# Kernel optimization log

Measured on AMD Instinct MI355X. Metric: run time of the kernel, lower is better.

The kernel has to match this reference:

```python
import jax, jax.numpy as jnp
import numpy as np

NUM_SEGMENTS = 4096  # number of graphs in the batch
E = 2097152          # number of edges
IN_CH = 64
HID_CH = 2 * IN_CH


def setup_inputs() -> dict:
    key = jax.random.key(0)
    k1, k2, k3, k4 = jax.random.split(key, 4)
    edge_attr = jax.random.normal(k1, (E, IN_CH), dtype=jnp.float32)
    batch = jnp.sort(jax.random.randint(k2, (E,), 0, NUM_SEGMENTS, dtype=jnp.int32))
    # MLP params: Linear(in, 2*in) -> ReLU -> Linear(2*in, 1)
    s1 = 1.0 / np.sqrt(IN_CH)
    s2 = 1.0 / np.sqrt(HID_CH)
    w1 = jax.random.uniform(k3, (IN_CH, HID_CH), jnp.float32, -s1, s1)
    b1 = jnp.zeros((HID_CH,), jnp.float32)
    w2 = jax.random.uniform(k4, (HID_CH, 1), jnp.float32, -s2, s2)
    b2 = jnp.zeros((1,), jnp.float32)
    return {"edge_attr": edge_attr, "w1": w1, "b1": b1, "w2": w2, "b2": b2, "batch": batch}


def reference(edge_attr, w1, b1, w2, b2, batch):
    # Tiny MLP scorer: [E, C] -> [E]
    h = jax.nn.relu(edge_attr @ w1 + b1)           # [E, 2C]
    score = (h @ w2 + b2).reshape(-1)              # [E]
    # Segment (per-graph) softmax keyed by `batch`, as in torch_geometric.utils.softmax
    seg_max = jax.ops.segment_max(score, batch, num_segments=NUM_SEGMENTS)  # [G]
    seg_max = jnp.where(jnp.isfinite(seg_max), seg_max, 0.0)  # empty segments
    ex = jnp.exp(score - seg_max[batch])           # [E]
    denom = jax.ops.segment_sum(ex, batch, num_segments=NUM_SEGMENTS)       # [G]
    return ex / (denom[batch] + 1e-16)
```

## Files before the change

kernel.cpp:

```cpp
#include <hip/hip_runtime.h>
#include <hip/hip_bf16.h>
#include <math.h>

typedef _Float16 half8  __attribute__((ext_vector_type(8)));
typedef __fp16   fp16x2 __attribute__((ext_vector_type(2)));
typedef float    floatx4 __attribute__((ext_vector_type(4)));

#define IN_CH 64
#define HID   128
#define NSEG  4096

__device__ __forceinline__ unsigned fkey(float s) {
    unsigned u = __float_as_uint(s);
    return (u & 0x80000000u) ? ~u : (u | 0x80000000u);
}
__device__ __forceinline__ float funkey(unsigned k) {
    unsigned u = (k & 0x80000000u) ? (k ^ 0x80000000u) : ~k;
    return __uint_as_float(u);
}

__global__ void init_seg(unsigned* __restrict__ segkey, float* __restrict__ denom) {
    int i = blockIdx.x * blockDim.x + threadIdx.x;
    if (i < NSEG) { segkey[i] = 0u; denom[i] = 0.0f; }
}

__global__ __launch_bounds__(256, 2) void mlp_score(
    const float* __restrict__ x, const float* __restrict__ w1,
    const float* __restrict__ b1, const float* __restrict__ w2,
    const float* __restrict__ b2, float* __restrict__ score, int E)
{
    __shared__ __align__(16) char smem[4 * 4 * 4096];

    const int tid  = threadIdx.x;
    const int lane = tid & 63;
    const int wid  = tid >> 6;
    const int g    = lane >> 4;
    const int l15  = lane & 15;
    const int ls4  = lane >> 4;

    half8 afr[2][8];
#pragma unroll
    for (int ks = 0; ks < 2; ++ks)
#pragma unroll
        for (int ct = 0; ct < 8; ++ct) {
            const float* wp = w1 + (size_t)(ks * 32 + g * 8) * HID + ct * 16 + l15;
            half8 h;
#pragma unroll
            for (int j = 0; j < 8; ++j) h[j] = (_Float16)wp[(size_t)j * HID];
            afr[ks][ct] = h;
        }

    floatx4 biasC[8], w2r[8];
#pragma unroll
    for (int ct = 0; ct < 8; ++ct)
#pragma unroll
        for (int r = 0; r < 4; ++r) {
            biasC[ct][r] = b1[ct * 16 + g * 4 + r];
            w2r[ct][r]   = w2[ct * 16 + g * 4 + r];
        }
    const float b2v = b2[0];

    const int nwtile = E >> 4;
    const int TOTW   = (int)gridDim.x * 4;
    const int gw     = blockIdx.x * 4 + wid;
    const int n      = nwtile / TOTW;
    const int rem    = nwtile - n * TOTW;

    char* lwave = smem + wid * 16384;
    const char* xb = (const char*)x;

    unsigned woff[4];
#pragma unroll
    for (int c = 0; c < 4; ++c) {
        int r = c * 4 + ls4;
        woff[c] = (unsigned)(r * 256 + ((l15 ^ r) & 15) * 16);
    }
    const unsigned roff = (unsigned)(l15 * 256 + (((2 * g) ^ l15) & 15) * 16);

    union H8 { half8 h8; fp16x2 h2[4]; };

#define STAGE(I) do {                                                          \
        size_t tb_ = (size_t)(gw + (I) * TOTW) * 4096;                         \
        char* lb_ = lwave + ((I) & 3) * 4096;                                  \
        __builtin_amdgcn_global_load_lds((const __attribute__((address_space(1))) void*)(xb + tb_ + woff[0]), (__attribute__((address_space(3))) void*)(lb_),        16, 0, 0); \
        __builtin_amdgcn_global_load_lds((const __attribute__((address_space(1))) void*)(xb + tb_ + woff[1]), (__attribute__((address_space(3))) void*)(lb_ + 1024), 16, 0, 0); \
        __builtin_amdgcn_global_load_lds((const __attribute__((address_space(1))) void*)(xb + tb_ + woff[2]), (__attribute__((address_space(3))) void*)(lb_ + 2048), 16, 0, 0); \
        __builtin_amdgcn_global_load_lds((const __attribute__((address_space(1))) void*)(xb + tb_ + woff[3]), (__attribute__((address_space(3))) void*)(lb_ + 3072), 16, 0, 0); \
    } while (0)

#define CORE(F0, F1, F2, F3, WT) do {                                          \
        H8 ub, uc;                                                             \
        ub.h2[0] = __builtin_amdgcn_cvt_pkrtz(F0[0], F0[1]);                   \
        ub.h2[1] = __builtin_amdgcn_cvt_pkrtz(F0[2], F0[3]);                   \
        ub.h2[2] = __builtin_amdgcn_cvt_pkrtz(F1[0], F1[1]);                   \
        ub.h2[3] = __builtin_amdgcn_cvt_pkrtz(F1[2], F1[3]);                   \
        uc.h2[0] = __builtin_amdgcn_cvt_pkrtz(F2[0], F2[1]);                   \
        uc.h2[1] = __builtin_amdgcn_cvt_pkrtz(F2[2], F2[3]);                   \
        uc.h2[2] = __builtin_amdgcn_cvt_pkrtz(F3[0], F3[1]);                   \
        uc.h2[3] = __builtin_amdgcn_cvt_pkrtz(F3[2], F3[3]);                   \
        floatx4 acc[8];                                                        \
        _Pragma("unroll")                                                      \
        for (int ct = 0; ct < 8; ++ct)                                         \
            acc[ct] = __builtin_amdgcn_mfma_f32_16x16x32_f16(afr[0][ct], ub.h8, biasC[ct], 0, 0, 0); \
        _Pragma("unroll")                                                      \
        for (int ct = 0; ct < 8; ++ct)                                         \
            acc[ct] = __builtin_amdgcn_mfma_f32_16x16x32_f16(afr[1][ct], uc.h8, acc[ct], 0, 0, 0);   \
        float s0 = 0.f, s1 = 0.f, s2 = 0.f, s3 = 0.f;                          \
        _Pragma("unroll")                                                      \
        for (int ct = 0; ct < 8; ++ct) {                                       \
            s0 += fmaxf(acc[ct][0], 0.f) * w2r[ct][0];                         \
            s1 += fmaxf(acc[ct][1], 0.f) * w2r[ct][1];                         \
            s2 += fmaxf(acc[ct][2], 0.f) * w2r[ct][2];                         \
            s3 += fmaxf(acc[ct][3], 0.f) * w2r[ct][3];                         \
        }                                                                      \
        float s = (s0 + s1) + (s2 + s3);                                       \
        s += __shfl_xor(s, 16);                                                \
        s += __shfl_xor(s, 32);                                                \
        if (lane < 16)                                                         \
            score[(size_t)(WT) * 16 + l15] = s + b2v;                          \
    } while (0)

#define BODY(I) do {                                                           \
        const char* lb_ = lwave + ((I) & 3) * 4096;                            \
        floatx4 f0 = *(const floatx4*)(lb_ + roff);                            \
        floatx4 f1 = *(const floatx4*)(lb_ + (roff ^ 16u));                    \
        floatx4 f2 = *(const floatx4*)(lb_ + (roff ^ 128u));                   \
        floatx4 f3 = *(const floatx4*)(lb_ + (roff ^ 144u));                   \
        CORE(f0, f1, f2, f3, gw + (I) * TOTW);                                 \
        __builtin_amdgcn_sched_barrier(0);                                     \
    } while (0)

    if (n >= 4) {
        STAGE(0); STAGE(1); STAGE(2);
        int i = 0;
        for (; i < n - 3; ++i) {
            STAGE(i + 3);
            asm volatile("s_waitcnt vmcnt(12)" ::: "memory");
            __builtin_amdgcn_sched_barrier(0);
            BODY(i);
        }
        asm volatile("s_waitcnt vmcnt(8)" ::: "memory");
        __builtin_amdgcn_sched_barrier(0);
        BODY(i); ++i;
        asm volatile("s_waitcnt vmcnt(4)" ::: "memory");
        __builtin_amdgcn_sched_barrier(0);
        BODY(i); ++i;
        asm volatile("s_waitcnt vmcnt(0)" ::: "memory");
        __builtin_amdgcn_sched_barrier(0);
        BODY(i);
    } else {
        for (int i = 0; i < n; ++i) {
            const float* xr = x + (size_t)(gw + i * TOTW) * (16 * IN_CH)
                                + (size_t)l15 * IN_CH + g * 8;
            floatx4 f0 = *(const floatx4*)(xr);
            floatx4 f1 = *(const floatx4*)(xr + 4);
            floatx4 f2 = *(const floatx4*)(xr + 32);
            floatx4 f3 = *(const floatx4*)(xr + 36);
            CORE(f0, f1, f2, f3, gw + i * TOTW);
        }
    }
    if (gw < rem) {
        int wt_ = n * TOTW + gw;
        const float* xr = x + (size_t)wt_ * (16 * IN_CH) + (size_t)l15 * IN_CH + g * 8;
        floatx4 f0 = *(const floatx4*)(xr);
        floatx4 f1 = *(const floatx4*)(xr + 4);
        floatx4 f2 = *(const floatx4*)(xr + 32);
        floatx4 f3 = *(const floatx4*)(xr + 36);
        CORE(f0, f1, f2, f3, wt_);
    }
#undef STAGE
#undef CORE
#undef BODY
}

__global__ __launch_bounds__(256) void seg_max(
    const float* __restrict__ score, const int* __restrict__ batch,
    unsigned* __restrict__ segkey, int E)
{
    int t = blockIdx.x * 256 + threadIdx.x;
    int i0 = t * 8;
    if (i0 + 8 > E) return;
    int4 bA = *(const int4*)(batch + i0);
    int4 bB = *(const int4*)(batch + i0 + 4);
    floatx4 sA = *(const floatx4*)(score + i0);
    floatx4 sB = *(const floatx4*)(score + i0 + 4);
    int   ids[8] = {bA.x, bA.y, bA.z, bA.w, bB.x, bB.y, bB.z, bB.w};
    float ss[8]  = {sA[0], sA[1], sA[2], sA[3], sB[0], sB[1], sB[2], sB[3]};
    int cur = ids[0];
    float m = ss[0];
#pragma unroll
    for (int j = 1; j < 8; ++j) {
        if (ids[j] == cur) {
            m = fmaxf(m, ss[j]);
        } else {
            atomicMax(segkey + cur, fkey(m));
            cur = ids[j];
            m = ss[j];
        }
    }
    atomicMax(segkey + cur, fkey(m));
}

__global__ __launch_bounds__(256) void seg_denom(
    const float* __restrict__ score, const int* __restrict__ batch,
    const unsigned* __restrict__ segkey, float* __restrict__ denom, int E)
{
    int t = blockIdx.x * 256 + threadIdx.x;
    int i0 = t * 8;
    if (i0 + 8 > E) return;
    int4 bA = *(const int4*)(batch + i0);
    int4 bB = *(const int4*)(batch + i0 + 4);
    floatx4 sA = *(const floatx4*)(score + i0);
    floatx4 sB = *(const floatx4*)(score + i0 + 4);
    int   ids[8] = {bA.x, bA.y, bA.z, bA.w, bB.x, bB.y, bB.z, bB.w};
    float ss[8]  = {sA[0], sA[1], sA[2], sA[3], sB[0], sB[1], sB[2], sB[3]};
    int cur = ids[0];
    float m = funkey(segkey[cur]);
    float a = __expf(ss[0] - m);
#pragma unroll
    for (int j = 1; j < 8; ++j) {
        if (ids[j] == cur) {
            a += __expf(ss[j] - m);
        } else {
            atomicAdd(denom + cur, a);
            cur = ids[j];
            m = funkey(segkey[cur]);
            a = __expf(ss[j] - m);
        }
    }
    atomicAdd(denom + cur, a);
}

__global__ __launch_bounds__(256) void finalize(
    float* __restrict__ score, const int* __restrict__ batch,
    const unsigned* __restrict__ segkey, const float* __restrict__ denom, int E)
{
    int t = blockIdx.x * 256 + threadIdx.x;
    int i0 = t * 8;
    if (i0 + 8 > E) return;
    int4 bA = *(const int4*)(batch + i0);
    int4 bB = *(const int4*)(batch + i0 + 4);
    floatx4 sA = *(const floatx4*)(score + i0);
    floatx4 sB = *(const floatx4*)(score + i0 + 4);
    int   ids[8] = {bA.x, bA.y, bA.z, bA.w, bB.x, bB.y, bB.z, bB.w};
    float ss[8]  = {sA[0], sA[1], sA[2], sA[3], sB[0], sB[1], sB[2], sB[3]};
    floatx4 oA, oB;
#pragma unroll
    for (int j = 0; j < 4; ++j) {
        float mj = funkey(segkey[ids[j]]);
        oA[j] = __expf(ss[j] - mj) / (denom[ids[j]] + 1e-16f);
    }
#pragma unroll
    for (int j = 0; j < 4; ++j) {
        float mj = funkey(segkey[ids[j + 4]]);
        oB[j] = __expf(ss[j + 4] - mj) / (denom[ids[j + 4]] + 1e-16f);
    }
    *(floatx4*)(score + i0)     = oA;
    *(floatx4*)(score + i0 + 4) = oB;
}

extern "C" void kernel_launch(void* const* d_in, const int* in_sizes, int n_in,
                              void* d_out, int out_size, void* d_ws, size_t ws_size,
                              hipStream_t stream) {
    const float* x   = (const float*)d_in[0];
    const float* w1  = (const float*)d_in[1];
    const float* b1  = (const float*)d_in[2];
    const float* w2  = (const float*)d_in[3];
    const float* b2  = (const float*)d_in[4];
    const int* batch = (const int*)d_in[5];
    float* out = (float*)d_out;
    const int E = in_sizes[5];

    unsigned* segkey = (unsigned*)d_ws;
    float*    denom  = (float*)((char*)d_ws + NSEG * sizeof(unsigned));

    init_seg<<<(NSEG + 255) / 256, 256, 0, stream>>>(segkey, denom);
    mlp_score<<<512, 256, 0, stream>>>(x, w1, b1, w2, b2, out, E);
    const int nthr = E / 8;
    seg_max   <<<nthr / 256, 256, 0, stream>>>(out, batch, segkey, E);
    seg_denom <<<nthr / 256, 256, 0, stream>>>(out, batch, segkey, denom, E);
    finalize  <<<nthr / 256, 256, 0, stream>>>(out, batch, segkey, denom, E);
}
```

Measured before the change: 196.6 us.

## Replace direct global-to-LDS loads with register-staged double-buffered pipeline

Swaps the global_load_lds asynchronous copies and vmcnt-based waits for ordinary global loads into two register sets, which are then written to swizzled LDS buffers. The main loop is unrolled by two and interleaves loads, LDS writes and MFMA bodies, with sched_group_barrier hints to pin the instruction order. The intent is better overlap of memory and compute and more scheduler control, at the cost of extra VGPRs and extra LDS write instructions. The fast path now requires an even tile count of at least six, with a simple per-tile fallback otherwise.

```diff
diff --git a/kernel.cpp b/kernel.cpp
--- a/kernel.cpp
+++ b/kernel.cpp
@@ -79,25 +79,34 @@
 
     union H8 { half8 h8; fp16x2 h2[4]; };
 
-#define STAGE(I) do {                                                          \
-        size_t tb_ = (size_t)(gw + (I) * TOTW) * 4096;                         \
-        char* lb_ = lwave + ((I) & 3) * 4096;                                  \
-        __builtin_amdgcn_global_load_lds((const __attribute__((address_space(1))) void*)(xb + tb_ + woff[0]), (__attribute__((address_space(3))) void*)(lb_),        16, 0, 0); \
-        __builtin_amdgcn_global_load_lds((const __attribute__((address_space(1))) void*)(xb + tb_ + woff[1]), (__attribute__((address_space(3))) void*)(lb_ + 1024), 16, 0, 0); \
-        __builtin_amdgcn_global_load_lds((const __attribute__((address_space(1))) void*)(xb + tb_ + woff[2]), (__attribute__((address_space(3))) void*)(lb_ + 2048), 16, 0, 0); \
-        __builtin_amdgcn_global_load_lds((const __attribute__((address_space(1))) void*)(xb + tb_ + woff[3]), (__attribute__((address_space(3))) void*)(lb_ + 3072), 16, 0, 0); \
-    } while (0)
-
-#define CORE(F0, F1, F2, F3, WT) do {                                          \
+#define TIDX(I) (gw + (I) * TOTW)
+
+#define LOADREG(F, T) do {                                                     \
+        const char* gs = xb + (size_t)(T) * 4096 + lane * 16;                  \
+        F##0 = *(const floatx4*)(gs);                                          \
+        F##1 = *(const floatx4*)(gs + 1024);                                   \
+        F##2 = *(const floatx4*)(gs + 2048);                                   \
+        F##3 = *(const floatx4*)(gs + 3072);                                   \
+    } while (0)
+
+#define WLDS(BI, F) do {                                                       \
+        char* lb_ = lwave + (BI) * 4096;                                       \
+        *(floatx4*)(lb_ + woff[0]) = F##0;                                     \
+        *(floatx4*)(lb_ + woff[1]) = F##1;                                     \
+        *(floatx4*)(lb_ + woff[2]) = F##2;                                     \
+        *(floatx4*)(lb_ + woff[3]) = F##3;                                     \
+    } while (0)
+
+#define CORE(F0_, F1_, F2_, F3_, WT) do {                                      \
         H8 ub, uc;                                                             \
-        ub.h2[0] = __builtin_amdgcn_cvt_pkrtz(F0[0], F0[1]);                   \
-        ub.h2[1] = __builtin_amdgcn_cvt_pkrtz(F0[2], F0[3]);                   \
-        ub.h2[2] = __builtin_amdgcn_cvt_pkrtz(F1[0], F1[1]);                   \
-        ub.h2[3] = __builtin_amdgcn_cvt_pkrtz(F1[2], F1[3]);                   \
-        uc.h2[0] = __builtin_amdgcn_cvt_pkrtz(F2[0], F2[1]);                   \
-        uc.h2[1] = __builtin_amdgcn_cvt_pkrtz(F2[2], F2[3]);                   \
-        uc.h2[2] = __builtin_amdgcn_cvt_pkrtz(F3[0], F3[1]);                   \
-        uc.h2[3] = __builtin_amdgcn_cvt_pkrtz(F3[2], F3[3]);                   \
+        ub.h2[0] = __builtin_amdgcn_cvt_pkrtz(F0_[0], F0_[1]);                 \
+        ub.h2[1] = __builtin_amdgcn_cvt_pkrtz(F0_[2], F0_[3]);                 \
+        ub.h2[2] = __builtin_amdgcn_cvt_pkrtz(F1_[0], F1_[1]);                 \
+        ub.h2[3] = __builtin_amdgcn_cvt_pkrtz(F1_[2], F1_[3]);                 \
+        uc.h2[0] = __builtin_amdgcn_cvt_pkrtz(F2_[0], F2_[1]);                 \
+        uc.h2[1] = __builtin_amdgcn_cvt_pkrtz(F2_[2], F2_[3]);                 \
+        uc.h2[2] = __builtin_amdgcn_cvt_pkrtz(F3_[0], F3_[1]);                 \
+        uc.h2[3] = __builtin_amdgcn_cvt_pkrtz(F3_[2], F3_[3]);                 \
         floatx4 acc[8];                                                        \
         _Pragma("unroll")                                                      \
         for (int ct = 0; ct < 8; ++ct)                                         \
@@ -126,51 +135,71 @@
         floatx4 f1 = *(const floatx4*)(lb_ + (roff ^ 16u));                    \
         floatx4 f2 = *(const floatx4*)(lb_ + (roff ^ 128u));                   \
         floatx4 f3 = *(const floatx4*)(lb_ + (roff ^ 144u));                   \
-        CORE(f0, f1, f2, f3, gw + (I) * TOTW);                                 \
-        __builtin_amdgcn_sched_barrier(0);                                     \
-    } while (0)
-
-    if (n >= 4) {
-        STAGE(0); STAGE(1); STAGE(2);
-        int i = 0;
-        for (; i < n - 3; ++i) {
-            STAGE(i + 3);
-            asm volatile("s_waitcnt vmcnt(12)" ::: "memory");
-            __builtin_amdgcn_sched_barrier(0);
+        CORE(f0, f1, f2, f3, TIDX(I));                                         \
+    } while (0)
+
+#define PIN() do {                                                             \
+        __builtin_amdgcn_sched_group_barrier(0x020, 4, 0);      \
+        __builtin_amdgcn_sched_group_barrier(0x100, 4, 0);       \
+        __builtin_amdgcn_sched_group_barrier(0x008, 16, 0);      \
+        __builtin_amdgcn_sched_group_barrier(0x200, 4, 0);       \
+    } while (0)
+
+    int i = 0;
+    if (n >= 6 && (n & 1) == 0) {
+        floatx4 P0, P1, P2, P3, Q0, Q1, Q2, Q3;
+        LOADREG(P, TIDX(0));
+        LOADREG(Q, TIDX(1));
+        WLDS(0, P);
+        LOADREG(P, TIDX(2));
+        WLDS(1, Q);
+        for (i = 0; i + 4 < n; i += 2) {
+            LOADREG(Q, TIDX(i + 3));
             BODY(i);
-        }
-        asm volatile("s_waitcnt vmcnt(8)" ::: "memory");
-        __builtin_amdgcn_sched_barrier(0);
-        BODY(i); ++i;
-        asm volatile("s_waitcnt vmcnt(4)" ::: "memory");
-        __builtin_amdgcn_sched_barrier(0);
-        BODY(i); ++i;
-        asm volatile("s_waitcnt vmcnt(0)" ::: "memory");
-        __builtin_amdgcn_sched_barrier(0);
+            WLDS((i + 2) & 3, P);
+            PIN();
+            LOADREG(P, TIDX(i + 4));
+            BODY(i + 1);
+            WLDS((i + 3) & 3, Q);
+            PIN();
+        }
+        LOADREG(Q, TIDX(n - 1));
+        BODY(n - 4);
+        WLDS((n - 2) & 3, P);
+        BODY(n - 3);
+        WLDS((n - 1) & 3, Q);
+        BODY(n - 2);
+        BODY(n - 1);
+        i = n;
+    }
+    for (; i < n; ++i) {
+        floatx4 P0, P1, P2, P3;
+        LOADREG(P, TIDX(i));
+        WLDS(i & 3, P);
         BODY(i);
-    } else {
-        for (int i = 0; i < n; ++i) {
-            const float* xr = x + (size_t)(gw + i * TOTW) * (16 * IN_CH)
-                                + (size_t)l15 * IN_CH + g * 8;
-            floatx4 f0 = *(const floatx4*)(xr);
-            floatx4 f1 = *(const floatx4*)(xr + 4);
-            floatx4 f2 = *(const floatx4*)(xr + 32);
-            floatx4 f3 = *(const floatx4*)(xr + 36);
-            CORE(f0, f1, f2, f3, gw + i * TOTW);
-        }
     }
     if (gw < rem) {
         int wt_ = n * TOTW + gw;
-        const float* xr = x + (size_t)wt_ * (16 * IN_CH) + (size_t)l15 * IN_CH + g * 8;
-        floatx4 f0 = *(const floatx4*)(xr);
-        floatx4 f1 = *(const floatx4*)(xr + 4);
-        floatx4 f2 = *(const floatx4*)(xr + 32);
-        floatx4 f3 = *(const floatx4*)(xr + 36);
+        floatx4 P0, P1, P2, P3;
+        const char* gs = xb + (size_t)wt_ * 4096 + lane * 16;
+        P0 = *(const floatx4*)(gs);
+        P1 = *(const floatx4*)(gs + 1024);
+        P2 = *(const floatx4*)(gs + 2048);
+        P3 = *(const floatx4*)(gs + 3072);
+        WLDS(0, P);
+        const char* lb_ = lwave;
+        floatx4 f0 = *(const floatx4*)(lb_ + roff);
+        floatx4 f1 = *(const floatx4*)(lb_ + (roff ^ 16u));
+        floatx4 f2 = *(const floatx4*)(lb_ + (roff ^ 128u));
+        floatx4 f3 = *(const floatx4*)(lb_ + (roff ^ 144u));
         CORE(f0, f1, f2, f3, wt_);
     }
-#undef STAGE
+#undef TIDX
+#undef LOADREG
+#undef WLDS
 #undef CORE
 #undef BODY
+#undef PIN
 }
 
 __global__ __launch_bounds__(256) void seg_max(
```

Measured after the change: 188.1 us. 4.3% less time.
